# Kernel tuning notes

Measured on AMD Instinct MI355X. Metric: run time of the kernel, lower is better.

## Reference

```python
import jax, jax.numpy as jnp
import numpy as np

NEG_SLOPE = 0.001

def _lrelu(v):
    return jnp.where(v > 0, v, NEG_SLOPE * v)

def _conv(x, w, pad):
    # x: NCHW, w: OIHW, stride 1
    return jax.lax.conv_general_dilated(
        x, w, window_strides=(1, 1), padding=[(pad, pad), (pad, pad)],
        dimension_numbers=("NCHW", "OIHW", "NCHW"))

def setup_inputs() -> dict:
    key = jax.random.key(0)
    ks = jax.random.split(key, 9)
    B, C, H, W = 16, 256, 160, 160
    x = jax.random.normal(ks[0], (B, C, H, W), dtype=jnp.float32)
    w1 = jax.random.normal(ks[1], (1, 2, 1, 1), dtype=jnp.float32) * 0.5
    w3 = jax.random.normal(ks[2], (1, 2, 3, 3), dtype=jnp.float32) * 0.2
    w5 = jax.random.normal(ks[3], (1, 2, 5, 5), dtype=jnp.float32) * 0.1
    w7 = jax.random.normal(ks[4], (1, 2, 7, 7), dtype=jnp.float32) * 0.07
    w_ab = jax.random.normal(ks[5], (1, 256, 1, 1), dtype=jnp.float32) * 0.06
    w_fc = jax.random.normal(ks[6], (1, 4, 1, 1), dtype=jnp.float32) * 0.5
    w_fd = jax.random.normal(ks[7], (256, 4, 1, 1), dtype=jnp.float32) * 0.5
    w_e = jax.random.normal(ks[8], (256, 256, 1, 1), dtype=jnp.float32) * 0.06
    return {"x": x, "w1": w1, "w3": w3, "w5": w5, "w7": w7,
            "w_ab": w_ab, "w_fc": w_fc, "w_fd": w_fd, "w_e": w_e}

def reference(x, w1, w3, w5, w7, w_ab, w_fc, w_fd, w_e):
    Bn, C, H, W = x.shape
    avg_out = jnp.mean(x, axis=1, keepdims=True)          # [B,1,H,W]
    max_out = jnp.max(x, axis=1, keepdims=True)           # [B,1,H,W]
    AM = jnp.concatenate([avg_out, max_out], axis=1)      # [B,2,H,W]
    S1 = _lrelu(_conv(AM, w1, 0))
    S3 = _lrelu(_conv(AM, w3, 1))
    S5 = _lrelu(_conv(AM, w5, 2))
    S7 = _lrelu(_conv(AM, w7, 3))
    Bm = _lrelu(_conv(x, w_ab, 0))                        # [B,1,H,W]
    F = jnp.concatenate([S1, S3, S5, S7], axis=1)         # [B,4,H,W]
    Cm = _lrelu(_conv(F, w_fc, 0))                        # [B,1,H,W]
    D = _lrelu(_conv(F, w_fd, 0))                         # [B,256,H,W]
    # faithful to torch: C[idx].view([W, H]) is a row-major RESHAPE, not transpose
    b2 = Bm[:, 0]                                          # [B,H,W]
    c2 = Cm[:, 0].reshape(Bn, W, H)                        # [B,W,H]
    S = jax.nn.softmax(jnp.einsum("bhw,bwk->bhk", b2, c2), axis=-1)  # [B,H,H]
    # S expanded over channels is identical per channel -> single einsum
    E = jnp.einsum("bhk,bckw->bchw", S, D)                 # [B,256,H,W]
    E = _conv(E, w_e, 0)
    return E + x
```

## Files before the change

kernel.cpp:

```cpp
#include <hip/hip_runtime.h>
#include <cstdint>
#include <cstddef>


#define SLOPE 0.001f
#define B_    16
#define C_    256
#define H_    160
#define W_    160
#define HW_   25600
#define NPIX_ 409600

__device__ __forceinline__ float lrelu(float v) { return v > 0.f ? v : SLOPE * v; }

__global__ void k_reduce(const float* __restrict__ x, const float* __restrict__ w_ab,
                         float* __restrict__ avg, float* __restrict__ mx,
                         float* __restrict__ bm) {
  int idx = blockIdx.x * 64 + threadIdx.x;
  int b   = idx / (HW_ / 4);
  int p4  = idx - b * (HW_ / 4);
  const float4* xb = (const float4*)x + (size_t)b * C_ * (HW_ / 4) + p4;
  float4 s = make_float4(0.f, 0.f, 0.f, 0.f);
  float4 m = make_float4(-INFINITY, -INFINITY, -INFINITY, -INFINITY);
  float4 d = make_float4(0.f, 0.f, 0.f, 0.f);
#pragma unroll 4
  for (int c = 0; c < C_; ++c) {
    float4 v = xb[(size_t)c * (HW_ / 4)];
    float  wc = w_ab[c];
    s.x += v.x; s.y += v.y; s.z += v.z; s.w += v.w;
    m.x = fmaxf(m.x, v.x); m.y = fmaxf(m.y, v.y);
    m.z = fmaxf(m.z, v.z); m.w = fmaxf(m.w, v.w);
    d.x = fmaf(wc, v.x, d.x); d.y = fmaf(wc, v.y, d.y);
    d.z = fmaf(wc, v.z, d.z); d.w = fmaf(wc, v.w, d.w);
  }
  int o4 = b * (HW_ / 4) + p4;
  const float inv = 1.f / (float)C_;
  ((float4*)avg)[o4] = make_float4(s.x * inv, s.y * inv, s.z * inv, s.w * inv);
  ((float4*)mx)[o4]  = m;
  ((float4*)bm)[o4]  = make_float4(lrelu(d.x), lrelu(d.y), lrelu(d.z), lrelu(d.w));
}

__global__ void k_convs(const float* __restrict__ avg, const float* __restrict__ mx,
                        const float* __restrict__ w1, const float* __restrict__ w3,
                        const float* __restrict__ w5, const float* __restrict__ w7,
                        const float* __restrict__ w_fc,
                        float* __restrict__ F, float* __restrict__ cm) {
  __shared__ float Aa[22][22];
  __shared__ float Am[22][22];
  int b = blockIdx.z, h0 = blockIdx.y * 16, w0 = blockIdx.x * 16;
  int t = threadIdx.x;
  const float* ab = avg + b * HW_;
  const float* mb = mx + b * HW_;
  for (int i = t; i < 22 * 22; i += 256) {
    int ih = i / 22, iw = i - ih * 22;
    int gh = h0 + ih - 3, gw = w0 + iw - 3;
    bool in = ((unsigned)gh < 160u) && ((unsigned)gw < 160u);
    Aa[ih][iw] = in ? ab[gh * 160 + gw] : 0.f;
    Am[ih][iw] = in ? mb[gh * 160 + gw] : 0.f;
  }
  __syncthreads();
  int ty = t >> 4, tx = t & 15;
  float s1 = w1[0] * Aa[ty + 3][tx + 3] + w1[1] * Am[ty + 3][tx + 3];
  float s3 = 0.f, s5 = 0.f, s7 = 0.f;
#pragma unroll
  for (int kh = 0; kh < 3; ++kh)
#pragma unroll
    for (int kw = 0; kw < 3; ++kw)
      s3 += w3[kh * 3 + kw] * Aa[ty + 2 + kh][tx + 2 + kw] +
            w3[9 + kh * 3 + kw] * Am[ty + 2 + kh][tx + 2 + kw];
#pragma unroll
  for (int kh = 0; kh < 5; ++kh)
#pragma unroll
    for (int kw = 0; kw < 5; ++kw)
      s5 += w5[kh * 5 + kw] * Aa[ty + 1 + kh][tx + 1 + kw] +
            w5[25 + kh * 5 + kw] * Am[ty + 1 + kh][tx + 1 + kw];
#pragma unroll
  for (int kh = 0; kh < 7; ++kh)
#pragma unroll
    for (int kw = 0; kw < 7; ++kw)
      s7 += w7[kh * 7 + kw] * Aa[ty + kh][tx + kw] +
            w7[49 + kh * 7 + kw] * Am[ty + kh][tx + kw];
  s1 = lrelu(s1); s3 = lrelu(s3); s5 = lrelu(s5); s7 = lrelu(s7);
  int hw = (h0 + ty) * 160 + (w0 + tx);
  F[(b * 4 + 0) * HW_ + hw] = s1;
  F[(b * 4 + 1) * HW_ + hw] = s3;
  F[(b * 4 + 2) * HW_ + hw] = s5;
  F[(b * 4 + 3) * HW_ + hw] = s7;
  cm[b * HW_ + hw] = lrelu(w_fc[0] * s1 + w_fc[1] * s3 + w_fc[2] * s5 + w_fc[3] * s7);
}

__global__ void k_attn(const float* __restrict__ bm, const float* __restrict__ cm,
                       float* __restrict__ S) {
  int h = blockIdx.x, b = blockIdx.y;
  int t = threadIdx.x;
  __shared__ float row[160];
  __shared__ float red[256];
  const float* bmr = bm + b * HW_ + h * 160;
  const float* cmb = cm + b * HW_;
  if (t < 160) row[t] = bmr[t];
  __syncthreads();
  float acc = 0.f;
  if (t < 160) {
    for (int w = 0; w < 160; ++w) acc = fmaf(row[w], cmb[w * 160 + t], acc);
  }
  red[t] = (t < 160) ? acc : -INFINITY;
  __syncthreads();
  for (int s = 128; s > 0; s >>= 1) {
    if (t < s) red[t] = fmaxf(red[t], red[t + s]);
    __syncthreads();
  }
  float mval = red[0];
  __syncthreads();
  float e = (t < 160) ? __expf(acc - mval) : 0.f;
  red[t] = e;
  __syncthreads();
  for (int s = 128; s > 0; s >>= 1) {
    if (t < s) red[t] += red[t + s];
    __syncthreads();
  }
  float inv = 1.f / red[0];
  if (t < 160) S[(b * 160 + h) * 160 + t] = e * inv;
}

__global__ __launch_bounds__(256) void k_gemm_g(
    const float* __restrict__ F, const float* __restrict__ w_fd,
    const float* __restrict__ w_e, float* __restrict__ G) {
  __shared__ float Fl[4][128];
  __shared__ float Wt[16][132];
  __shared__ float Dt[16][132];
  int bx = blockIdx.x;
  int b  = bx / 200;
  int p0 = (bx - b * 200) * 128;
  int ot0 = blockIdx.y * 128;
  int t = threadIdx.x, tx = t & 15, ty = t >> 4;
  for (int i = t; i < 512; i += 256) {
    int j = i >> 7, pp = i & 127;
    Fl[j][pp] = F[(b * 4 + j) * HW_ + p0 + pp];
  }
  float acc[8][8];
#pragma unroll
  for (int i = 0; i < 8; ++i)
#pragma unroll
    for (int j = 0; j < 8; ++j) acc[i][j] = 0.f;

  for (int ct = 0; ct < 256; ct += 16) {
    __syncthreads();
#pragma unroll
    for (int i = t; i < 2048; i += 256) {
      int o = i >> 4, cc = i & 15;
      Wt[cc][o] = w_e[(ot0 + o) * 256 + ct + cc];
    }
#pragma unroll
    for (int i = t; i < 2048; i += 256) {
      int cc = i >> 7, pp = i & 127;
      const float* fd = w_fd + (ct + cc) * 4;
      float v = fd[0] * Fl[0][pp] + fd[1] * Fl[1][pp] +
                fd[2] * Fl[2][pp] + fd[3] * Fl[3][pp];
      Dt[cc][pp] = lrelu(v);
    }
    __syncthreads();
#pragma unroll
    for (int kk = 0; kk < 16; ++kk) {
      float aR[8], bR[8];
#pragma unroll
      for (int i = 0; i < 8; ++i) aR[i] = Wt[kk][ty + 16 * i];
#pragma unroll
      for (int j = 0; j < 8; ++j) bR[j] = Dt[kk][tx + 16 * j];
#pragma unroll
      for (int i = 0; i < 8; ++i)
#pragma unroll
        for (int j = 0; j < 8; ++j) acc[i][j] = fmaf(aR[i], bR[j], acc[i][j]);
    }
  }
#pragma unroll
  for (int i = 0; i < 8; ++i) {
    int o = ot0 + ty + 16 * i;
    float* row = G + ((size_t)(b * 256 + o)) * HW_ + p0;
#pragma unroll
    for (int j = 0; j < 8; ++j) row[tx + 16 * j] = acc[i][j];
  }
}

__global__ __launch_bounds__(256) void k_out_f(
    const float* __restrict__ S, const float* __restrict__ x,
    float* __restrict__ out) {
  __shared__ float Gp[80 * 160];
  __shared__ float St[160 * 17];
  int bo = blockIdx.x;
  int b  = bo >> 8;
  int t = threadIdx.x, tx = t & 15, ty = t >> 4;
  const float* g  = out + (size_t)bo * HW_;
  const float* Sb = S + b * HW_;
  float acc[10][10];
#pragma unroll
  for (int i = 0; i < 10; ++i)
#pragma unroll
    for (int j = 0; j < 10; ++j) acc[i][j] = 0.f;
  int h0 = ty * 10, w0 = tx * 10;

  for (int half = 0; half < 2; ++half) {
    __syncthreads();
    for (int i = t; i < 80 * 160; i += 256) Gp[i] = g[half * 12800 + i];
    for (int kt = 0; kt < 80; kt += 16) {
      __syncthreads();
      for (int i = t; i < 2560; i += 256) {
        int hh = i >> 4, kk = i & 15;
        St[hh * 17 + kk] = Sb[hh * 160 + half * 80 + kt + kk];
      }
      __syncthreads();
#pragma unroll
      for (int kk = 0; kk < 16; ++kk) {
        float aR[10], bR[10];
#pragma unroll
        for (int i = 0; i < 10; ++i) aR[i] = St[(h0 + i) * 17 + kk];
#pragma unroll
        for (int j = 0; j < 10; ++j) bR[j] = Gp[(kt + kk) * 160 + w0 + j];
#pragma unroll
        for (int i = 0; i < 10; ++i)
#pragma unroll
          for (int j = 0; j < 10; ++j) acc[i][j] = fmaf(aR[i], bR[j], acc[i][j]);
      }
    }
  }
  const float* xb = x + (size_t)bo * HW_;
  float* ob = out + (size_t)bo * HW_;
#pragma unroll
  for (int i = 0; i < 10; ++i) {
    int h = h0 + i;
#pragma unroll
    for (int j = 0; j < 10; ++j)
      ob[h * 160 + w0 + j] = acc[i][j] + xb[h * 160 + w0 + j];
  }
}

extern "C" void kernel_launch(void* const* d_in, const int* in_sizes, int n_in,
                              void* d_out, int out_size, void* d_ws, size_t ws_size,
                              hipStream_t stream) {
  const float* x    = (const float*)d_in[0];
  const float* w1   = (const float*)d_in[1];
  const float* w3   = (const float*)d_in[2];
  const float* w5   = (const float*)d_in[3];
  const float* w7   = (const float*)d_in[4];
  const float* w_ab = (const float*)d_in[5];
  const float* w_fc = (const float*)d_in[6];
  const float* w_fd = (const float*)d_in[7];
  const float* w_e  = (const float*)d_in[8];
  float* out = (float*)d_out;

  float* ws  = (float*)d_ws;
  float* avg = ws;
  float* mx  = ws + 409600;
  float* bm  = ws + 819200;
  float* Fb  = ws + 1228800;
  float* cm  = ws + 2867200;
  float* Sm  = ws + 3276800;

  k_reduce<<<NPIX_ / 4 / 64, 64, 0, stream>>>(x, w_ab, avg, mx, bm);
  k_convs<<<dim3(10, 10, 16), 256, 0, stream>>>(avg, mx, w1, w3, w5, w7, w_fc, Fb, cm);
  k_attn<<<dim3(160, 16), 256, 0, stream>>>(bm, cm, Sm);
  k_gemm_g<<<dim3(3200, 2), 256, 0, stream>>>(Fb, w_fd, w_e, out);
  k_out_f<<<4096, 256, 0, stream>>>(Sm, x, out);
}
```

Before: 2.751 ms.

## Reorder matmuls: apply softmax to D first, then channel-mix with w_e

Swaps the order of the two large contractions. Each (b,c) plane of D is now recomputed on the fly from F and multiplied by S first, then the 256x256 w_e channel mix and the residual add run as a separate GEMM over pixel tiles, using a pre-transposed w_e and float4 loads. The old kernel rebuilt D inside the channel GEMM and staged whole planes in shared memory for the S multiply. The FLOP count is unchanged, but memory access and occupancy differ, and the intermediate still makes a full round trip through the output buffer.

```diff
diff --git a/kernel.cpp b/kernel.cpp
--- a/kernel.cpp
+++ b/kernel.cpp
@@ -122,115 +122,128 @@
   if (t < 160) S[(b * 160 + h) * 160 + t] = e * inv;
 }
 
-__global__ __launch_bounds__(256) void k_gemm_g(
-    const float* __restrict__ F, const float* __restrict__ w_fd,
-    const float* __restrict__ w_e, float* __restrict__ G) {
-  __shared__ float Fl[4][128];
-  __shared__ float Wt[16][132];
-  __shared__ float Dt[16][132];
-  int bx = blockIdx.x;
-  int b  = bx / 200;
-  int p0 = (bx - b * 200) * 128;
-  int ot0 = blockIdx.y * 128;
+__global__ void k_wt(const float* __restrict__ w_e, float* __restrict__ w_eT) {
+  int c = blockIdx.x;
+  int o = threadIdx.x;
+  w_eT[c * 256 + o] = w_e[o * 256 + c];
+}
+
+__global__ __launch_bounds__(256, 3) void k_smm(
+    const float* __restrict__ S, const float* __restrict__ F,
+    const float* __restrict__ w_fd, float* __restrict__ E0) {
+  __shared__ float St[160 * 16];
+  __shared__ float Dt[16 * 160];
+  int c = blockIdx.x, b = blockIdx.y;
   int t = threadIdx.x, tx = t & 15, ty = t >> 4;
-  for (int i = t; i < 512; i += 256) {
-    int j = i >> 7, pp = i & 127;
-    Fl[j][pp] = F[(b * 4 + j) * HW_ + p0 + pp];
-  }
-  float acc[8][8];
-#pragma unroll
-  for (int i = 0; i < 8; ++i)
-#pragma unroll
-    for (int j = 0; j < 8; ++j) acc[i][j] = 0.f;
+  float wf[4];
+  *(float4*)wf = *(const float4*)(w_fd + c * 4);
+  const float* Sb = S + b * HW_;
+  const float* Fb = F + (size_t)b * 4 * HW_;
+  float acc[10][10];
+#pragma unroll
+  for (int i = 0; i < 10; ++i)
+#pragma unroll
+    for (int j = 0; j < 10; ++j) acc[i][j] = 0.f;
+
+  for (int kt = 0; kt < 160; kt += 16) {
+    __syncthreads();
+    for (int i = t; i < 640; i += 256) {
+      int h = i >> 2, c4 = (i & 3) << 2;
+      *(float4*)(St + h * 16 + c4) = *(const float4*)(Sb + h * 160 + kt + c4);
+    }
+    for (int i = t; i < 640; i += 256) {
+      int kk = i / 40, w4 = (i - kk * 40) << 2;
+      const float* fp = Fb + (kt + kk) * 160 + w4;
+      float f0[4], f1[4], f2[4], f3[4], d[4];
+      *(float4*)f0 = *(const float4*)(fp);
+      *(float4*)f1 = *(const float4*)(fp + HW_);
+      *(float4*)f2 = *(const float4*)(fp + 2 * HW_);
+      *(float4*)f3 = *(const float4*)(fp + 3 * HW_);
+#pragma unroll
+      for (int q = 0; q < 4; ++q)
+        d[q] = lrelu(wf[0] * f0[q] + wf[1] * f1[q] + wf[2] * f2[q] + wf[3] * f3[q]);
+      *(float4*)(Dt + kk * 160 + w4) = *(float4*)d;
+    }
+    __syncthreads();
+#pragma unroll 4
+    for (int kk = 0; kk < 16; ++kk) {
+      float aR[10], bR[10];
+#pragma unroll
+      for (int i = 0; i < 10; ++i) aR[i] = St[(ty + 16 * i) * 16 + kk];
+#pragma unroll
+      for (int j = 0; j < 10; ++j) bR[j] = Dt[kk * 160 + tx + 16 * j];
+#pragma unroll
+      for (int i = 0; i < 10; ++i)
+#pragma unroll
+        for (int j = 0; j < 10; ++j) acc[i][j] = fmaf(aR[i], bR[j], acc[i][j]);
+    }
+  }
+  float* Eb = E0 + ((size_t)(b * 256 + c)) * HW_;
+#pragma unroll
+  for (int i = 0; i < 10; ++i) {
+    int h = ty + 16 * i;
+#pragma unroll
+    for (int j = 0; j < 10; ++j) Eb[h * 160 + tx + 16 * j] = acc[i][j];
+  }
+}
+
+__global__ __launch_bounds__(256, 4) void k_emm(
+    const float* __restrict__ w_eT, const float* __restrict__ x,
+    float* __restrict__ out) {
+  __shared__ float Wt[16 * 256];
+  __shared__ float Et[16 * 64];
+  int px0 = blockIdx.x * 64, b = blockIdx.y;
+  int t = threadIdx.x, tx = t & 15, ty = t >> 4;
+  float acc[16][4];
+#pragma unroll
+  for (int i = 0; i < 16; ++i)
+#pragma unroll
+    for (int j = 0; j < 4; ++j) acc[i][j] = 0.f;
+  const float* Eb = out + (size_t)b * 256 * HW_ + px0;
 
   for (int ct = 0; ct < 256; ct += 16) {
     __syncthreads();
-#pragma unroll
-    for (int i = t; i < 2048; i += 256) {
-      int o = i >> 4, cc = i & 15;
-      Wt[cc][o] = w_e[(ot0 + o) * 256 + ct + cc];
-    }
-#pragma unroll
-    for (int i = t; i < 2048; i += 256) {
-      int cc = i >> 7, pp = i & 127;
-      const float* fd = w_fd + (ct + cc) * 4;
-      float v = fd[0] * Fl[0][pp] + fd[1] * Fl[1][pp] +
-                fd[2] * Fl[2][pp] + fd[3] * Fl[3][pp];
-      Dt[cc][pp] = lrelu(v);
+    *(float4*)(Et + ty * 64 + tx * 4) =
+        *(const float4*)(Eb + (size_t)(ct + ty) * HW_ + tx * 4);
+#pragma unroll
+    for (int r = 0; r < 4; ++r) {
+      int idx = t + 256 * r;
+      int cc = idx >> 6, o4 = (idx & 63) << 2;
+      *(float4*)(Wt + cc * 256 + o4) =
+          *(const float4*)(w_eT + (ct + cc) * 256 + o4);
     }
     __syncthreads();
 #pragma unroll
     for (int kk = 0; kk < 16; ++kk) {
-      float aR[8], bR[8];
-#pragma unroll
-      for (int i = 0; i < 8; ++i) aR[i] = Wt[kk][ty + 16 * i];
-#pragma unroll
-      for (int j = 0; j < 8; ++j) bR[j] = Dt[kk][tx + 16 * j];
-#pragma unroll
-      for (int i = 0; i < 8; ++i)
-#pragma unroll
-        for (int j = 0; j < 8; ++j) acc[i][j] = fmaf(aR[i], bR[j], acc[i][j]);
-    }
-  }
-#pragma unroll
-  for (int i = 0; i < 8; ++i) {
-    int o = ot0 + ty + 16 * i;
-    float* row = G + ((size_t)(b * 256 + o)) * HW_ + p0;
-#pragma unroll
-    for (int j = 0; j < 8; ++j) row[tx + 16 * j] = acc[i][j];
-  }
-}
-
-__global__ __launch_bounds__(256) void k_out_f(
-    const float* __restrict__ S, const float* __restrict__ x,
-    float* __restrict__ out) {
-  __shared__ float Gp[80 * 160];
-  __shared__ float St[160 * 17];
-  int bo = blockIdx.x;
-  int b  = bo >> 8;
-  int t = threadIdx.x, tx = t & 15, ty = t >> 4;
-  const float* g  = out + (size_t)bo * HW_;
-  const float* Sb = S + b * HW_;
-  float acc[10][10];
-#pragma unroll
-  for (int i = 0; i < 10; ++i)
-#pragma unroll
-    for (int j = 0; j < 10; ++j) acc[i][j] = 0.f;
-  int h0 = ty * 10, w0 = tx * 10;
-
-  for (int half = 0; half < 2; ++half) {
-    __syncthreads();
-    for (int i = t; i < 80 * 160; i += 256) Gp[i] = g[half * 12800 + i];
-    for (int kt = 0; kt < 80; kt += 16) {
-      __syncthreads();
-      for (int i = t; i < 2560; i += 256) {
-        int hh = i >> 4, kk = i & 15;
-        St[hh * 17 + kk] = Sb[hh * 160 + half * 80 + kt + kk];
-      }
-      __syncthreads();
-#pragma unroll
-      for (int kk = 0; kk < 16; ++kk) {
-        float aR[10], bR[10];
-#pragma unroll
-        for (int i = 0; i < 10; ++i) aR[i] = St[(h0 + i) * 17 + kk];
-#pragma unroll
-        for (int j = 0; j < 10; ++j) bR[j] = Gp[(kt + kk) * 160 + w0 + j];
-#pragma unroll
-        for (int i = 0; i < 10; ++i)
-#pragma unroll
-          for (int j = 0; j < 10; ++j) acc[i][j] = fmaf(aR[i], bR[j], acc[i][j]);
-      }
-    }
-  }
-  const float* xb = x + (size_t)bo * HW_;
-  float* ob = out + (size_t)bo * HW_;
-#pragma unroll
-  for (int i = 0; i < 10; ++i) {
-    int h = h0 + i;
-#pragma unroll
-    for (int j = 0; j < 10; ++j)
-      ob[h * 160 + w0 + j] = acc[i][j] + xb[h * 160 + w0 + j];
-  }
+      float e[4], wv[4][4];
+      *(float4*)e = *(const float4*)(Et + kk * 64 + tx * 4);
+#pragma unroll
+      for (int g = 0; g < 4; ++g)
+        *(float4*)wv[g] = *(const float4*)(Wt + kk * 256 + ty * 4 + 64 * g);
+#pragma unroll
+      for (int g = 0; g < 4; ++g)
+#pragma unroll
+        for (int oo = 0; oo < 4; ++oo)
+#pragma unroll
+          for (int p = 0; p < 4; ++p)
+            acc[g * 4 + oo][p] = fmaf(wv[g][oo], e[p], acc[g * 4 + oo][p]);
+    }
+  }
+  const float* xb = x + (size_t)b * 256 * HW_ + px0;
+  float* ob = out + (size_t)b * 256 * HW_ + px0;
+#pragma unroll
+  for (int g = 0; g < 4; ++g)
+#pragma unroll
+    for (int oo = 0; oo < 4; ++oo) {
+      int o = ty * 4 + 64 * g + oo;
+      float4 xv = *(const float4*)(xb + (size_t)o * HW_ + tx * 4);
+      float4 rv;
+      rv.x = acc[g * 4 + oo][0] + xv.x;
+      rv.y = acc[g * 4 + oo][1] + xv.y;
+      rv.z = acc[g * 4 + oo][2] + xv.z;
+      rv.w = acc[g * 4 + oo][3] + xv.w;
+      *(float4*)(ob + (size_t)o * HW_ + tx * 4) = rv;
+    }
 }
 
 extern "C" void kernel_launch(void* const* d_in, const int* in_sizes, int n_in,
@@ -254,10 +267,12 @@
   float* Fb  = ws + 1228800;
   float* cm  = ws + 2867200;
   float* Sm  = ws + 3276800;
+  float* weT = avg;
 
   k_reduce<<<NPIX_ / 4 / 64, 64, 0, stream>>>(x, w_ab, avg, mx, bm);
   k_convs<<<dim3(10, 10, 16), 256, 0, stream>>>(avg, mx, w1, w3, w5, w7, w_fc, Fb, cm);
+  k_wt<<<256, 256, 0, stream>>>(w_e, weT);
   k_attn<<<dim3(160, 16), 256, 0, stream>>>(bm, cm, Sm);
-  k_gemm_g<<<dim3(3200, 2), 256, 0, stream>>>(Fb, w_fd, w_e, out);
-  k_out_f<<<4096, 256, 0, stream>>>(Sm, x, out);
-}
+  k_smm<<<dim3(256, 16), 256, 0, stream>>>(Sm, Fb, w_fd, out);
+  k_emm<<<dim3(400, 16), 256, 0, stream>>>(weT, x, out);
+}
```

Result: no change. 2.723 ms (-1.0%).
